# Kernel tuning notes

Measured on AMD Instinct MI355X. Metric: run time of the kernel, lower is better.

The kernel has to match this reference:

```python
import jax, jax.numpy as jnp
import numpy as np

B, S = 64, 512
VOCAB, D, H, NH = 50000, 256, 256, 4
MAX_DUR = 12.0
SCALE_RATE = 1.0


def setup_inputs() -> dict:
    key = jax.random.key(0)
    ks = jax.random.split(key, 12)
    s = 1.0 / np.sqrt(H)
    inp = {
        "src": jax.random.randint(ks[0], (B, S), 0, VOCAB),
        "input_len": jax.random.randint(ks[1], (B,), 1, S + 1),
        "fix_src": jax.random.uniform(ks[2], (B, S), jnp.float32) * MAX_DUR,
        "emb_table": jax.random.normal(ks[3], (VOCAB, D), jnp.float32) * 0.02,
        "Wi": jax.random.uniform(ks[4], (H, D), jnp.float32, -s, s),
        "bi": jax.random.uniform(ks[5], (H,), jnp.float32, -s, s),
        "Wh": jax.random.uniform(ks[6], (H, NH * H), jnp.float32, -s, s),
        "bh": jax.random.uniform(ks[7], (H,), jnp.float32, -s, s),
        "fc1_W": jax.random.uniform(ks[8], (D, NH * H), jnp.float32, -s, s),
        "fc1_b": jax.random.uniform(ks[9], (D,), jnp.float32, -s, s),
        "fc2_W": jax.random.uniform(ks[10], (2, D), jnp.float32, -s, s),
        "fc2_b": jax.random.uniform(ks[11], (2,), jnp.float32, -s, s),
    }
    return inp


def _forward(src, input_len, fix_src, emb_table, Wi, bi, Wh, bh, fc1_W, fc1_b, fc2_W, fc2_b):
    emb = emb_table[src]                      # [B, S, D]
    offsets = jnp.arange(NH, dtype=emb.dtype) * (MAX_DUR / NH)  # [NH]
    h0 = jnp.zeros((NH, B, H), emb.dtype)

    def step(h, xd):
        x, d = xd                             # x [B,D], d [B]
        hcat = jnp.swapaxes(h, 0, 1).reshape(B, NH * H)
        cand = jnp.tanh(x @ Wi.T + bi + hcat @ Wh.T + bh)        # [B,H]
        g = jax.nn.sigmoid(d[:, None] * SCALE_RATE - offsets)    # [B,NH]
        gt = g.T[:, :, None]                                     # [NH,B,1]
        h_new = gt * cand[None, :, :] + (1.0 - gt) * h           # [NH,B,H]
        out = jnp.swapaxes(h_new, 0, 1).reshape(B, NH * H)
        return h_new, out

    xs = (jnp.swapaxes(emb, 0, 1), fix_src.T)  # [S,B,D], [S,B]
    _, outs = jax.lax.scan(step, h0, xs)       # [S, B, NH*H]
    outs = jnp.swapaxes(outs, 0, 1)            # [B, S, NH*H]
    sel = outs[jnp.arange(B), input_len - 1]   # gather at last valid step, [B, NH*H]
    hid = jnp.tanh(sel @ fc1_W.T + fc1_b)      # [B, D]
    return hid @ fc2_W.T + fc2_b               # [B, 2]


def reference(src, input_len, fix_src, emb_table, Wi, bi, Wh, bh, fc1_W, fc1_b, fc2_W, fc2_b):
    return _forward(src, input_len, fix_src, emb_table, Wi, bi, Wh, bh, fc1_W, fc1_b, fc2_W, fc2_b)
```

## Files before the change

kernel.cpp:

```cpp
#include <hip/hip_runtime.h>
#include <stdint.h>

constexpr int BB = 64;
constexpr int SS = 512;
constexpr int DD = 256;
constexpr int HH = 256;
constexpr int NHH = 4;
constexpr int KK = 1024;

constexpr int TT = 512;

typedef _Float16 f16;
typedef _Float16 f16x2 __attribute__((ext_vector_type(2)));
typedef _Float16 half8 __attribute__((ext_vector_type(8)));
typedef float f32x4 __attribute__((ext_vector_type(4)));

__device__ inline float dot2p(uint32_t a, uint32_t b, float c) {
  f16x2 av = __builtin_bit_cast(f16x2, a);
  f16x2 bv = __builtin_bit_cast(f16x2, b);
#if defined(__has_builtin)
#if __has_builtin(__builtin_amdgcn_fdot2)
  return __builtin_amdgcn_fdot2(av, bv, c, false);
#else
  return c + (float)av.x * (float)bv.x + (float)av.y * (float)bv.y;
#endif
#else
  return c + (float)av.x * (float)bv.x + (float)av.y * (float)bv.y;
#endif
}

__device__ inline float dot8(uint4 w, uint4 a, float c) {
  c = dot2p(w.x, a.x, c);
  c = dot2p(w.y, a.y, c);
  c = dot2p(w.z, a.z, c);
  c = dot2p(w.w, a.w, c);
  return c;
}

__device__ inline uint32_t pack2(float a, float b) {
  f16x2 v;
  v.x = (f16)a;
  v.y = (f16)b;
  return __builtin_bit_cast(uint32_t, v);
}

__device__ inline float fast_tanh(float x) {
  x = fminf(fmaxf(x, -15.f), 15.f);
  float e = __expf(2.f * x);
  return 1.f - 2.f / (e + 1.f);
}

__global__ void k_pack_wq(const float* __restrict__ Wh, uint4* __restrict__ Wq) {
  int gid = blockIdx.x * blockDim.x + threadIdx.x;
  int p = gid >> 13;
  int m = (gid >> 9) & 15;
  int t = gid & 511;
  int j = m >> 2, u = m & 3;
  int wv = t >> 6, l = t & 63;
  const float* s = Wh + (size_t)(64 * p + l) * KK + 256 * j + 32 * wv + 8 * u;
  uint4 w;
  w.x = pack2(s[0], s[1]);
  w.y = pack2(s[2], s[3]);
  w.z = pack2(s[4], s[5]);
  w.w = pack2(s[6], s[7]);
  Wq[gid] = w;
}

__global__ void k_transpose8(const float* __restrict__ src, float* __restrict__ dst,
                             int C, int total) {
  int gid = blockIdx.x * blockDim.x + threadIdx.x;
  if (gid >= total) return;
  int r = gid & 255, c = gid >> 8;
  dst[gid] = src[r * C + c];
}

__global__ void k_cvt_f16(const float* __restrict__ src, f16* __restrict__ dst,
                          int total) {
  int gid = blockIdx.x * blockDim.x + threadIdx.x;
  if (gid >= total) return;
  dst[gid] = (f16)src[gid];
}

__global__ __launch_bounds__(256) void k_u_mfma(
    const int* __restrict__ src, const float* __restrict__ emb,
    const f16* __restrict__ wif, const float* __restrict__ bi,
    const float* __restrict__ bh, const int* __restrict__ input_len,
    f16* __restrict__ U) {
  __shared__ __align__(16) char xls[32768];
  const int row0 = blockIdx.x * 64;
  const int b = row0 >> 9;
  if ((row0 & 511) >= input_len[b]) return;
  const int t = threadIdx.x;
  const int w = t >> 6, l = t & 63;

  for (int rr = 0; rr < 16; ++rr) {
    int r = w * 16 + rr;
    int srcid = src[row0 + r];
    const float4 x = *(const float4*)(emb + (size_t)srcid * DD + l * 4);
    uint2 dw;
    dw.x = pack2(x.x, x.y);
    dw.y = pack2(x.z, x.w);
    int byte = (r * 512 + l * 8) ^ ((r & 7) << 4);
    *(uint2*)(xls + byte) = dw;
  }
  __syncthreads();

  const int lm = l & 15, lk = l >> 4;
  const int arow = w * 16 + lm;
  const int xs = (arow & 7) << 4;

  for (int ct = 0; ct < 16; ++ct) {
    const int o = ct * 16 + lm;
    f32x4 acc = {0.f, 0.f, 0.f, 0.f};
    const f16* bp = wif + (size_t)o * 256 + lk * 8;
#pragma unroll
    for (int kt = 0; kt < 8; ++kt) {
      int ab = (arow * 512 + kt * 64 + lk * 16) ^ xs;
      half8 af = *(const half8*)(xls + ab);
      half8 bf = *(const half8*)(bp + kt * 32);
      acc = __builtin_amdgcn_mfma_f32_16x16x32_f16(af, bf, acc, 0, 0, 0);
    }
    float bias = bi[o] + bh[o];
#pragma unroll
    for (int reg = 0; reg < 4; ++reg) {
      int grow = row0 + w * 16 + lk * 4 + reg;
      U[(size_t)grow * HH + o] = (f16)(acc[reg] + bias);
    }
  }
}

__global__ void __attribute__((amdgpu_flat_work_group_size(512, 512),
                               amdgpu_waves_per_eu(2, 2)))
k_recurrence(
    const uint4* __restrict__ Wq, const f16* __restrict__ U,
    const float* __restrict__ fix_src, const int* __restrict__ input_len,
    const float* __restrict__ fc1T, const float* __restrict__ fc1_b,
    const float* __restrict__ fc2_W, const float* __restrict__ fc2_b,
    float* __restrict__ out, uint32_t* __restrict__ Cex,
    float* __restrict__ FPg, int* __restrict__ Flg) {
  __shared__ __align__(16) char arena[61440];
  f16* cbuf = (f16*)arena;
  uint4* cvec = (uint4*)arena;
  float* part = (float*)(arena + 512);
  float* partials = (float*)(arena + 512);
  float* hbuf = (float*)(arena + 8704);

  const int idx = blockIdx.x;
  const int b = idx & 63;
  const int p = idx >> 6;
  const int t = threadIdx.x;
  const int out_i = t & 255, ch2 = t >> 8;
  const int n = out_i >> 6, o_loc = out_i & 63;
  const int wv = t >> 6, l = t & 63;

  uint4 w[16];
  {
    const uint4* wp = Wq + (p * 16) * TT + t;
#pragma unroll
    for (int m = 0; m < 16; ++m) {
      const uint4* a = wp + m * TT;
      asm volatile("global_load_dwordx4 %0, %1, off"
                   : "=v"(w[m]) : "v"(a) : "memory");
    }
    asm volatile("s_waitcnt vmcnt(0)" ::: "memory");
  }

  float v0 = 0.f, v1 = 0.f, v2 = 0.f, v3 = 0.f;
  float h = 0.f;

  const int len = input_len[b];
  const f16* Ub = U + (size_t)b * SS * HH;
  const float* fsb = fix_src + b * SS;

  if (t < 64) {
    float c0 = fast_tanh((float)Ub[64 * p + t]);
    f16 chv = (f16)c0;
    cbuf[64 * p + t] = chv;
    uint32_t dwp =
        ((uint32_t)__builtin_bit_cast(unsigned short, chv) << 16) | 1u;
    __hip_atomic_store(&Cex[b * 256 + p * 64 + t], dwp, __ATOMIC_RELAXED,
                       __HIP_MEMORY_SCOPE_AGENT);
  }

#pragma unroll 1
  for (int s = 0; s < len; ++s) {
#pragma unroll
    for (int m = 0; m < 16; ++m)
      asm volatile("" : "+v"(w[m].x), "+v"(w[m].y), "+v"(w[m].z), "+v"(w[m].w));

    const int par = s & 1;
    const uint32_t tag = (uint32_t)((s + 1) & 0xffff);
    const float dval = fsb[s];
    float g = 0.f, gq1 = 0.f, gq2 = 0.f, gq3 = 0.f, ufn = 0.f;

    if (t < 64) {
      int sn = (s + 1 < len) ? (s + 1) : s;
      ufn = (float)Ub[(size_t)sn * HH + 64 * p + t];
      g   = 1.f / (1.f + __expf(0.f - dval));
      gq1 = 1.f / (1.f + __expf(3.f - dval));
      gq2 = 1.f / (1.f + __expf(6.f - dval));
      gq3 = 1.f / (1.f + __expf(9.f - dval));
    } else if (t < 256) {
      g = 1.f / (1.f + __expf((float)(3 * n) - dval));
      int wvp = t >> 6;
      int lane = t & 63;
      int q = (p + wvp) & 3;
      const int off = ((par * 64 + b) * 4 + q) * 64 + lane;
      uint32_t dw;
      do {
        dw = __hip_atomic_load(&Cex[off], __ATOMIC_RELAXED,
                               __HIP_MEMORY_SCOPE_AGENT);
      } while ((dw & 0xffffu) != tag);
      cbuf[64 * q + lane] =
          __builtin_bit_cast(f16, (unsigned short)(dw >> 16));
    }
    __syncthreads();

    {
      const uint4* ap = cvec + 4 * wv;
      uint4 a0 = ap[0], a1 = ap[1], a2 = ap[2], a3 = ap[3];
      float ac0 = 0.f, ac1 = 0.f, ac2 = 0.f, ac3 = 0.f;
      ac0 = dot8(w[0], a0, ac0);  ac0 = dot8(w[1], a1, ac0);
      ac0 = dot8(w[2], a2, ac0);  ac0 = dot8(w[3], a3, ac0);
      ac1 = dot8(w[4], a0, ac1);  ac1 = dot8(w[5], a1, ac1);
      ac1 = dot8(w[6], a2, ac1);  ac1 = dot8(w[7], a3, ac1);
      ac2 = dot8(w[8], a0, ac2);  ac2 = dot8(w[9], a1, ac2);
      ac2 = dot8(w[10], a2, ac2); ac2 = dot8(w[11], a3, ac2);
      ac3 = dot8(w[12], a0, ac3); ac3 = dot8(w[13], a1, ac3);
      ac3 = dot8(w[14], a2, ac3); ac3 = dot8(w[15], a3, ac3);
      part[wv * 256 +   0 + l] = ac0;
      part[wv * 256 +  64 + l] = ac1;
      part[wv * 256 + 128 + l] = ac2;
      part[wv * 256 + 192 + l] = ac3;
    }

    if (t < 256) {
      float cown = (float)cbuf[64 * p + o_loc];
      h = g * cown + (1.f - g) * h;
    }
    __syncthreads();

    if (t < 64) {
      float w0 = 0.f, w1 = 0.f, w2 = 0.f, w3 = 0.f;
#pragma unroll
      for (int kc = 0; kc < 8; ++kc) {
        const float* pr = part + kc * 256;
        w0 += pr[t];
        w1 += pr[64 + t];
        w2 += pr[128 + t];
        w3 += pr[192 + t];
      }
      v0 = g   * w0 + (1.f - g)   * v0;
      v1 = gq1 * w1 + (1.f - gq1) * v1;
      v2 = gq2 * w2 + (1.f - gq2) * v2;
      v3 = gq3 * w3 + (1.f - gq3) * v3;
      float c = fast_tanh(ufn + (v0 + v1 + v2 + v3));
      f16 chv = (f16)c;
      uint32_t dwp =
          ((uint32_t)__builtin_bit_cast(unsigned short, chv) << 16) |
          (uint32_t)((s + 2) & 0xffff);
      const int po = (((s + 1) & 1) * 64 + b) * 256 + p * 64 + t;
      __hip_atomic_store(&Cex[po], dwp, __ATOMIC_RELAXED,
                         __HIP_MEMORY_SCOPE_AGENT);
      cbuf[64 * p + t] = chv;
    }
  }

  if (t < 256) hbuf[out_i] = h;
  __syncthreads();
  {
    float acc = 0.f;
#pragma unroll 4
    for (int r = 0; r < 128; ++r) {
      int k_loc = ch2 * 128 + r;
      int n2 = k_loc >> 6, il = k_loc & 63;
      int kg = n2 * 256 + 64 * p + il;
      acc += hbuf[k_loc] * fc1T[(size_t)kg * 256 + out_i];
    }
    partials[t] = acc;
  }
  __syncthreads();
  if (t < 256) FPg[(b * 4 + p) * 256 + out_i] =
      partials[out_i] + partials[256 + out_i];
  __syncthreads();
  if (t == 0)
    __hip_atomic_store(&Flg[b * 4 + p], 0x5A5A5A5A, __ATOMIC_RELEASE,
                       __HIP_MEMORY_SCOPE_AGENT);
  if (p != 0) return;
  if (t < 4 && t > 0) {
    while (__hip_atomic_load(&Flg[b * 4 + t], __ATOMIC_ACQUIRE,
                             __HIP_MEMORY_SCOPE_AGENT) != 0x5A5A5A5A) {
    }
  }
  __syncthreads();
  if (t < 256) {
    float pre = fc1_b[t];
#pragma unroll
    for (int q = 0; q < 4; ++q)
      pre += __hip_atomic_load(&FPg[(b * 4 + q) * 256 + t], __ATOMIC_RELAXED,
                               __HIP_MEMORY_SCOPE_AGENT);
    hbuf[t] = fast_tanh(pre);
  }
  __syncthreads();
  if (t < 64) {
    float p0 = 0.f, p1 = 0.f;
    for (int oi = t; oi < 256; oi += 64) {
      float hh = hbuf[oi];
      p0 += hh * fc2_W[oi];
      p1 += hh * fc2_W[256 + oi];
    }
#pragma unroll
    for (int off = 32; off; off >>= 1) {
      p0 += __shfl_down(p0, off);
      p1 += __shfl_down(p1, off);
    }
    if (t == 0) {
      out[b * 2 + 0] = p0 + fc2_b[0];
      out[b * 2 + 1] = p1 + fc2_b[1];
    }
  }
}

extern "C" void kernel_launch(void* const* d_in, const int* in_sizes, int n_in,
                              void* d_out, int out_size, void* d_ws, size_t ws_size,
                              hipStream_t stream) {
  const int* src = (const int*)d_in[0];
  const int* input_len = (const int*)d_in[1];
  const float* fix_src = (const float*)d_in[2];
  const float* emb = (const float*)d_in[3];
  const float* Wi = (const float*)d_in[4];
  const float* bi = (const float*)d_in[5];
  const float* Wh = (const float*)d_in[6];
  const float* bh = (const float*)d_in[7];
  const float* fc1_W = (const float*)d_in[8];
  const float* fc1_b = (const float*)d_in[9];
  const float* fc2_W = (const float*)d_in[10];
  const float* fc2_b = (const float*)d_in[11];
  float* out = (float*)d_out;

  char* ws = (char*)d_ws;
  uint4* Wq = (uint4*)(ws);
  f16* wif = (f16*)(ws + (512ull << 10));
  float* fc1T = (float*)(ws + (768ull << 10));
  f16* U = (f16*)(ws + (1792ull << 10));
  uint32_t* Cex = (uint32_t*)(ws + (18176ull << 10));
  float* FPg = (float*)(ws + (18304ull << 10));
  int* Flg = (int*)(ws + (18560ull << 10));
  const size_t needed = (18561ull << 10);
  if (ws_size < needed) return;

  k_pack_wq<<<128, 256, 0, stream>>>(Wh, Wq);
  k_cvt_f16<<<(65536 + 255) / 256, 256, 0, stream>>>(Wi, wif, 65536);
  k_transpose8<<<(262144 + 255) / 256, 256, 0, stream>>>(fc1_W, fc1T, 1024, 262144);
  k_u_mfma<<<BB * SS / 64, 256, 0, stream>>>(src, emb, wif, bi, bh,
                                             input_len, U);
  k_recurrence<<<BB * 4, TT, 0, stream>>>(Wq, U, fix_src, input_len, fc1T,
                                          fc1_b, fc2_W, fc2_b, out, Cex, FPg,
                                          Flg);
}
```

Baseline: 721.6 us.

## Remove one block barrier per step via double-buffered partials and chunk remapping

Each wave now owns a fixed 32-element chunk of the exchanged candidate vector. Wave 0 keeps its own chunk locally and the other waves poll only the chunk they consume, so the barrier between the exchange and the dot products is gone. The partial-sum buffer is double-buffered by step parity so one __syncthreads per step is enough, and the Wh packing is permuted to match the new chunk order. Gate math and the h state updates move into wave 0 and fix_src is staged into LDS. The risk is read/write races on the shared cbuf across steps, and wave 0 carries more serial work per step.

```diff
diff --git a/kernel.cpp b/kernel.cpp
--- a/kernel.cpp
+++ b/kernel.cpp
@@ -50,6 +50,12 @@
   return 1.f - 2.f / (e + 1.f);
 }
 
+__device__ __host__ inline int chunk_of(int p, int wv) {
+  if (wv == 0) return 2 * p;
+  if (wv == 7) return 2 * p + 1;
+  return (2 * p + 1 + wv) & 7;
+}
+
 __global__ void k_pack_wq(const float* __restrict__ Wh, uint4* __restrict__ Wq) {
   int gid = blockIdx.x * blockDim.x + threadIdx.x;
   int p = gid >> 13;
@@ -57,7 +63,8 @@
   int t = gid & 511;
   int j = m >> 2, u = m & 3;
   int wv = t >> 6, l = t & 63;
-  const float* s = Wh + (size_t)(64 * p + l) * KK + 256 * j + 32 * wv + 8 * u;
+  int cw = chunk_of(p, wv);
+  const float* s = Wh + (size_t)(64 * p + l) * KK + 256 * j + 32 * cw + 8 * u;
   uint4 w;
   w.x = pack2(s[0], s[1]);
   w.y = pack2(s[2], s[3]);
@@ -139,19 +146,22 @@
     float* __restrict__ out, uint32_t* __restrict__ Cex,
     float* __restrict__ FPg, int* __restrict__ Flg) {
   __shared__ __align__(16) char arena[61440];
-  f16* cbuf = (f16*)arena;
-  uint4* cvec = (uint4*)arena;
+  f16* cbufX = (f16*)arena;
+  uint4* cvecX = (uint4*)arena;
   float* part = (float*)(arena + 512);
   float* partials = (float*)(arena + 512);
-  float* hbuf = (float*)(arena + 8704);
+  float* hbuf = (float*)(arena + 16896);
+  float* fsbuf = (float*)(arena + 17920);
 
   const int idx = blockIdx.x;
   const int b = idx & 63;
   const int p = idx >> 6;
   const int t = threadIdx.x;
+  const int wv = t >> 6, l = t & 63;
   const int out_i = t & 255, ch2 = t >> 8;
-  const int n = out_i >> 6, o_loc = out_i & 63;
-  const int wv = t >> 6, l = t & 63;
+
+  const int cw = chunk_of(p, wv);
+  const int q = cw >> 1, half = cw & 1;
 
   uint4 w[16];
   {
@@ -166,21 +176,25 @@
   }
 
   float v0 = 0.f, v1 = 0.f, v2 = 0.f, v3 = 0.f;
-  float h = 0.f;
+  float h0 = 0.f, h1 = 0.f, h2 = 0.f, h3 = 0.f;
+  float cprev = 0.f, unew = 0.f;
 
   const int len = input_len[b];
   const f16* Ub = U + (size_t)b * SS * HH;
   const float* fsb = fix_src + b * SS;
 
-  if (t < 64) {
-    float c0 = fast_tanh((float)Ub[64 * p + t]);
+  fsbuf[t] = fsb[t];
+  if (wv == 0) {
+    float c0 = fast_tanh((float)Ub[64 * p + l]);
     f16 chv = (f16)c0;
-    cbuf[64 * p + t] = chv;
+    cprev = (float)chv;
+    if (l < 32) cbufX[2 * p * 32 + l] = chv;
     uint32_t dwp =
         ((uint32_t)__builtin_bit_cast(unsigned short, chv) << 16) | 1u;
-    __hip_atomic_store(&Cex[b * 256 + p * 64 + t], dwp, __ATOMIC_RELAXED,
+    __hip_atomic_store(&Cex[b * 256 + p * 64 + l], dwp, __ATOMIC_RELAXED,
                        __HIP_MEMORY_SCOPE_AGENT);
   }
+  __syncthreads();
 
 #pragma unroll 1
   for (int s = 0; s < len; ++s) {
@@ -190,34 +204,34 @@
 
     const int par = s & 1;
     const uint32_t tag = (uint32_t)((s + 1) & 0xffff);
-    const float dval = fsb[s];
-    float g = 0.f, gq1 = 0.f, gq2 = 0.f, gq3 = 0.f, ufn = 0.f;
-
-    if (t < 64) {
+    float g0 = 0.f, g1 = 0.f, g2 = 0.f, g3 = 0.f;
+
+    if (wv == 0) {
+      const float dval = fsbuf[s];
+      g0 = 1.f / (1.f + __expf(0.f - dval));
+      g1 = 1.f / (1.f + __expf(3.f - dval));
+      g2 = 1.f / (1.f + __expf(6.f - dval));
+      g3 = 1.f / (1.f + __expf(9.f - dval));
+      h0 = g0 * cprev + (1.f - g0) * h0;
+      h1 = g1 * cprev + (1.f - g1) * h1;
+      h2 = g2 * cprev + (1.f - g2) * h2;
+      h3 = g3 * cprev + (1.f - g3) * h3;
       int sn = (s + 1 < len) ? (s + 1) : s;
-      ufn = (float)Ub[(size_t)sn * HH + 64 * p + t];
-      g   = 1.f / (1.f + __expf(0.f - dval));
-      gq1 = 1.f / (1.f + __expf(3.f - dval));
-      gq2 = 1.f / (1.f + __expf(6.f - dval));
-      gq3 = 1.f / (1.f + __expf(9.f - dval));
-    } else if (t < 256) {
-      g = 1.f / (1.f + __expf((float)(3 * n) - dval));
-      int wvp = t >> 6;
-      int lane = t & 63;
-      int q = (p + wvp) & 3;
-      const int off = ((par * 64 + b) * 4 + q) * 64 + lane;
-      uint32_t dw;
-      do {
-        dw = __hip_atomic_load(&Cex[off], __ATOMIC_RELAXED,
-                               __HIP_MEMORY_SCOPE_AGENT);
-      } while ((dw & 0xffffu) != tag);
-      cbuf[64 * q + lane] =
-          __builtin_bit_cast(f16, (unsigned short)(dw >> 16));
-    }
-    __syncthreads();
+      unew = (float)Ub[(size_t)sn * HH + 64 * p + l];
+    } else {
+      if (l < 32) {
+        uint32_t* addr = &Cex[((par * 64 + b) * 4 + q) * 64 + 32 * half + l];
+        uint32_t dw;
+        do {
+          dw = __hip_atomic_load(addr, __ATOMIC_RELAXED,
+                                 __HIP_MEMORY_SCOPE_AGENT);
+        } while ((dw & 0xffffu) != tag);
+        cbufX[cw * 32 + l] = __builtin_bit_cast(f16, (unsigned short)(dw >> 16));
+      }
+    }
 
     {
-      const uint4* ap = cvec + 4 * wv;
+      const uint4* ap = cvecX + cw * 4;
       uint4 a0 = ap[0], a1 = ap[1], a2 = ap[2], a3 = ap[3];
       float ac0 = 0.f, ac1 = 0.f, ac2 = 0.f, ac3 = 0.f;
       ac0 = dot8(w[0], a0, ac0);  ac0 = dot8(w[1], a1, ac0);
@@ -228,45 +242,47 @@
       ac2 = dot8(w[10], a2, ac2); ac2 = dot8(w[11], a3, ac2);
       ac3 = dot8(w[12], a0, ac3); ac3 = dot8(w[13], a1, ac3);
       ac3 = dot8(w[14], a2, ac3); ac3 = dot8(w[15], a3, ac3);
-      part[wv * 256 +   0 + l] = ac0;
-      part[wv * 256 +  64 + l] = ac1;
-      part[wv * 256 + 128 + l] = ac2;
-      part[wv * 256 + 192 + l] = ac3;
-    }
-
-    if (t < 256) {
-      float cown = (float)cbuf[64 * p + o_loc];
-      h = g * cown + (1.f - g) * h;
+      float* pr = part + par * 2048 + cw * 256;
+      pr[l] = ac0;
+      pr[64 + l] = ac1;
+      pr[128 + l] = ac2;
+      pr[192 + l] = ac3;
     }
     __syncthreads();
 
-    if (t < 64) {
-      float w0 = 0.f, w1 = 0.f, w2 = 0.f, w3 = 0.f;
+    if (wv == 0) {
+      float s0 = 0.f, s1 = 0.f, s2 = 0.f, s3 = 0.f;
+      const float* pb = part + par * 2048;
 #pragma unroll
       for (int kc = 0; kc < 8; ++kc) {
-        const float* pr = part + kc * 256;
-        w0 += pr[t];
-        w1 += pr[64 + t];
-        w2 += pr[128 + t];
-        w3 += pr[192 + t];
+        const float* pr = pb + kc * 256;
+        s0 += pr[l];
+        s1 += pr[64 + l];
+        s2 += pr[128 + l];
+        s3 += pr[192 + l];
       }
-      v0 = g   * w0 + (1.f - g)   * v0;
-      v1 = gq1 * w1 + (1.f - gq1) * v1;
-      v2 = gq2 * w2 + (1.f - gq2) * v2;
-      v3 = gq3 * w3 + (1.f - gq3) * v3;
-      float c = fast_tanh(ufn + (v0 + v1 + v2 + v3));
+      v0 = g0 * s0 + (1.f - g0) * v0;
+      v1 = g1 * s1 + (1.f - g1) * v1;
+      v2 = g2 * s2 + (1.f - g2) * v2;
+      v3 = g3 * s3 + (1.f - g3) * v3;
+      float c = fast_tanh(unew + (v0 + v1 + v2 + v3));
       f16 chv = (f16)c;
+      cprev = (float)chv;
       uint32_t dwp =
           ((uint32_t)__builtin_bit_cast(unsigned short, chv) << 16) |
           (uint32_t)((s + 2) & 0xffff);
-      const int po = (((s + 1) & 1) * 64 + b) * 256 + p * 64 + t;
-      __hip_atomic_store(&Cex[po], dwp, __ATOMIC_RELAXED,
-                         __HIP_MEMORY_SCOPE_AGENT);
-      cbuf[64 * p + t] = chv;
-    }
-  }
-
-  if (t < 256) hbuf[out_i] = h;
+      __hip_atomic_store(&Cex[(((s + 1) & 1) * 64 + b) * 256 + p * 64 + l],
+                         dwp, __ATOMIC_RELAXED, __HIP_MEMORY_SCOPE_AGENT);
+      if (l < 32) cbufX[2 * p * 32 + l] = chv;
+    }
+  }
+
+  if (wv == 0) {
+    hbuf[l] = h0;
+    hbuf[64 + l] = h1;
+    hbuf[128 + l] = h2;
+    hbuf[192 + l] = h3;
+  }
   __syncthreads();
   {
     float acc = 0.f;
@@ -296,8 +312,8 @@
   if (t < 256) {
     float pre = fc1_b[t];
 #pragma unroll
-    for (int q = 0; q < 4; ++q)
-      pre += __hip_atomic_load(&FPg[(b * 4 + q) * 256 + t], __ATOMIC_RELAXED,
+    for (int qq = 0; qq < 4; ++qq)
+      pre += __hip_atomic_load(&FPg[(b * 4 + qq) * 256 + t], __ATOMIC_RELAXED,
                                __HIP_MEMORY_SCOPE_AGENT);
     hbuf[t] = fast_tanh(pre);
   }
```

Measured after the change: 704.7 us. 2.3% less time.
